# Optimization experiments

Measured on AMD Instinct MI355X. Metric: run time of the kernel, lower is better.

Reference implementation:

```python
import jax, jax.numpy as jnp
import numpy as np

TOP_K = 2
EPS = 1e-9


def setup_inputs() -> dict:
    key = jax.random.key(0)
    k1, k2, k3, k4 = jax.random.split(key, 4)
    B, T, D, H, E = 4, 2048, 1024, 4096, 8
    x = jax.random.normal(k1, (B, T, D), dtype=jnp.float32)
    Wr = jax.random.normal(k2, (D, E), dtype=jnp.float32) * 0.02
    W1 = jax.random.normal(k3, (E, D, H), dtype=jnp.float32) * 0.02
    W2 = jax.random.normal(k4, (E, H, D), dtype=jnp.float32) * 0.02
    return {"x": x, "Wr": Wr, "W1": W1, "W2": W2}


def reference(x, Wr, W1, W2):
    # x: (B,T,D); Wr: (D,E); W1: (E,D,H); W2: (E,H,D)
    E = Wr.shape[1]
    logits = jnp.einsum('btd,de->bte', x, Wr)          # (B,T,E)
    probs = jax.nn.softmax(logits, axis=-1)
    top_p, top_i = jax.lax.top_k(probs, TOP_K)         # (B,T,K)
    gates = top_p / (jnp.sum(top_p, axis=-1, keepdims=True) + EPS)
    # combine weights per expert: (B,T,E), zero where expert not selected
    oh = jax.nn.one_hot(top_i, E, dtype=x.dtype)       # (B,T,K,E)
    comb = jnp.sum(oh * gates[..., None], axis=2)      # (B,T,E)
    out = jnp.zeros_like(x)
    for e in range(E):  # fixed small expert loop
        h = jax.nn.gelu(jnp.einsum('btd,dh->bth', x, W1[e]), approximate=False)
        y = jnp.einsum('bth,hd->btd', h, W2[e])
        out = out + comb[..., e:e + 1] * y
    # load-balancing loss (on detached stats, matching torch .detach())
    mask = (jnp.sum(oh, axis=2) > 0).astype(jnp.float32)  # (B,T,E)
    imp = jnp.sum(jax.lax.stop_gradient(probs), axis=(0, 1))
    load = jnp.sum(jax.lax.stop_gradient(mask), axis=(0, 1))
    imp = imp / (jnp.sum(imp) + EPS)
    load = load / (jnp.sum(load) + EPS)
    lb = jnp.sum(imp * load) * E
    return out, lb
```

## Files before the change

kernel.cpp:

```cpp
#include <hip/hip_runtime.h>
#include <hip/hip_bf16.h>
#include <math.h>

#define NTOK 8192
#define DDIM 1024
#define HDIM 4096
#define NEXP 8
#define HROWS (NTOK*2 + 128)
#define RBLK 512

typedef unsigned int u32;
typedef unsigned short u16;
typedef __bf16 bf16x8 __attribute__((ext_vector_type(8)));
typedef float f32x4 __attribute__((ext_vector_type(4)));
typedef u16 u16x8 __attribute__((ext_vector_type(8)));
typedef u16 u16x4 __attribute__((ext_vector_type(4)));

__device__ __forceinline__ u16 f2bf(float f){
  u32 u = __builtin_bit_cast(u32, f);
  u32 r = (u + 0x7FFFu + ((u >> 16) & 1u)) >> 16;
  return (u16)r;
}
__device__ __forceinline__ float bf2f(u16 b){
  u32 u = ((u32)b) << 16;
  return __builtin_bit_cast(float, u);
}
__device__ __forceinline__ void gl_lds16(const void* g, void* l){
  __builtin_amdgcn_global_load_lds(
      (const __attribute__((address_space(1))) u32*)g,
      (__attribute__((address_space(3))) u32*)l, 16, 0, 0);
}

__global__ __launch_bounds__(256) void cvtx_kernel(const float* __restrict__ x,
                                                   u16* __restrict__ xb){
  long i = (long)(blockIdx.x * 256 + threadIdx.x) * 8;
  float4 a = *(const float4*)(x + i);
  float4 b = *(const float4*)(x + i + 4);
  u16x8 o;
  o[0]=f2bf(a.x); o[1]=f2bf(a.y); o[2]=f2bf(a.z); o[3]=f2bf(a.w);
  o[4]=f2bf(b.x); o[5]=f2bf(b.y); o[6]=f2bf(b.z); o[7]=f2bf(b.w);
  *(u16x8*)(xb + i) = o;
}

__global__ __launch_bounds__(256) void transpose_cvt(const float* __restrict__ in,
                                                     u16* __restrict__ out,
                                                     int R, int C){
  int e = blockIdx.z;
  const float* pin = in + (long)e * R * C;
  u16* pout = out + (long)e * R * C;
  __shared__ u16 tile[64][65];
  int c0 = blockIdx.x * 64, r0 = blockIdx.y * 64;
  int tid = threadIdx.x;
#pragma unroll
  for (int j = 0; j < 16; j++){
    int idx = tid + 256 * j;
    int r = idx >> 6, c = idx & 63;
    tile[r][c] = f2bf(pin[(long)(r0 + r) * C + c0 + c]);
  }
  __syncthreads();
#pragma unroll
  for (int j = 0; j < 16; j++){
    int idx = tid + 256 * j;
    int r = idx >> 6, c = idx & 63;
    pout[(long)(c0 + r) * R + r0 + c] = tile[c][r];
  }
}

__global__ __launch_bounds__(1024) void route_kernel(const float* __restrict__ x,
                                                     const float* __restrict__ Wr,
                                                     int4* __restrict__ meta,
                                                     float2* __restrict__ gates,
                                                     int* __restrict__ selrk,
                                                     int* __restrict__ blockhist,
                                                     float* __restrict__ impPart){
  const int wid = threadIdx.x >> 6;
  const int lane = threadIdx.x & 63;
  const int t = blockIdx.x * 16 + wid;
  const float* xr = x + (long)t * DDIM;
  float acc[NEXP] = {};
  for (int d0 = lane * 4; d0 < DDIM; d0 += 256){
    float4 xv = *(const float4*)(xr + d0);
    const float* w = Wr + d0 * NEXP;
#pragma unroll
    for (int q = 0; q < 4; q++){
      float xq = ((const float*)&xv)[q];
      float4 w0 = *(const float4*)(w + q * NEXP);
      float4 w1 = *(const float4*)(w + q * NEXP + 4);
      acc[0] += xq * w0.x; acc[1] += xq * w0.y; acc[2] += xq * w0.z; acc[3] += xq * w0.w;
      acc[4] += xq * w1.x; acc[5] += xq * w1.y; acc[6] += xq * w1.z; acc[7] += xq * w1.w;
    }
  }
#pragma unroll
  for (int e = 0; e < NEXP; e++){
#pragma unroll
    for (int off = 32; off; off >>= 1) acc[e] += __shfl_xor(acc[e], off, 64);
  }
  __shared__ int sel_s[32];
  __shared__ float p_s[16][NEXP];
  if (lane == 0){
    float mx = acc[0];
#pragma unroll
    for (int e = 1; e < NEXP; e++) mx = fmaxf(mx, acc[e]);
    float p[NEXP]; float s = 0.f;
#pragma unroll
    for (int e = 0; e < NEXP; e++){ p[e] = expf(acc[e] - mx); s += p[e]; }
    float inv = 1.f / s;
#pragma unroll
    for (int e = 0; e < NEXP; e++){ p[e] *= inv; p_s[wid][e] = p[e]; }
    int i0 = 0; float v0 = p[0];
#pragma unroll
    for (int e = 1; e < NEXP; e++) if (p[e] > v0){ v0 = p[e]; i0 = e; }
    int i1 = -1; float v1 = -1.f;
#pragma unroll
    for (int e = 0; e < NEXP; e++) if (e != i0 && p[e] > v1){ v1 = p[e]; i1 = e; }
    float gs = v0 + v1 + 1e-9f;
    meta[t] = make_int4(i0, i1, 0, 0);
    gates[t] = make_float2(v0 / gs, v1 / gs);
    sel_s[wid * 2] = i0;
    sel_s[wid * 2 + 1] = i1;
  }
  __syncthreads();
  const int tid = threadIdx.x;
  if (tid < 32){
    int e = sel_s[tid];
    int r = 0;
    for (int m = 0; m < tid; m++) r += (sel_s[m] == e) ? 1 : 0;
    selrk[blockIdx.x * 32 + tid] = (r << 3) | e;
  }
  if (tid < NEXP){
    int hcount = 0;
#pragma unroll
    for (int m = 0; m < 32; m++) hcount += (sel_s[m] == tid) ? 1 : 0;
    blockhist[blockIdx.x * NEXP + tid] = hcount;
    float s = 0.f;
#pragma unroll
    for (int w = 0; w < 16; w++) s += p_s[w][tid];
    impPart[blockIdx.x * NEXP + tid] = s;
  }
}

__global__ __launch_bounds__(512) void scan_kernel(int* __restrict__ blockhist,
                                                   const float* __restrict__ impPart,
                                                   int* __restrict__ cnt,
                                                   int* __restrict__ offs,
                                                   float* __restrict__ imp){
  const int e = threadIdx.x >> 6;
  const int lane = threadIdx.x & 63;
  const int base = lane * 8;
  int v[8]; int s = 0;
#pragma unroll
  for (int i = 0; i < 8; i++){
    int tmp = blockhist[(base + i) * NEXP + e];
    v[i] = s; s += tmp;
  }
  int inc = s;
#pragma unroll
  for (int off = 1; off < 64; off <<= 1){
    int o = __shfl_up(inc, off, 64);
    if (lane >= off) inc += o;
  }
  int excl = inc - s;
#pragma unroll
  for (int i = 0; i < 8; i++) blockhist[(base + i) * NEXP + e] = v[i] + excl;
  int tot = __shfl(inc, 63, 64);
  float fs = 0.f;
#pragma unroll
  for (int i = 0; i < 8; i++) fs += impPart[(base + i) * NEXP + e];
#pragma unroll
  for (int off = 32; off; off >>= 1) fs += __shfl_xor(fs, off, 64);
  __shared__ int cnt_s[NEXP];
  if (lane == 0){ cnt_s[e] = tot; cnt[e] = tot; imp[e] = fs; }
  __syncthreads();
  if (threadIdx.x == 0){
    int o = 0;
    for (int q = 0; q < NEXP; q++){ offs[q] = o; o += cnt_s[q]; }
  }
}

__global__ __launch_bounds__(256) void fill_kernel(const int* __restrict__ selrk,
                                                   const int* __restrict__ blockhist,
                                                   int* __restrict__ elist,
                                                   int4* __restrict__ meta){
  int m = blockIdx.x * 256 + threadIdx.x;
  int t = m >> 1, c = m & 1, b = m >> 5;
  int pk = selrk[m];
  int e = pk & 7, r = pk >> 3;
  int gslot = blockhist[b * NEXP + e] + r;
  elist[e * NTOK + gslot] = t;
  ((int*)meta)[t * 4 + 2 + c] = gslot;
}

__global__ __launch_bounds__(256) void gemm1_kernel(const u16* __restrict__ xb,
                                                    const u16* __restrict__ w1t,
                                                    u16* __restrict__ h,
                                                    const int* __restrict__ elist,
                                                    const int* __restrict__ cnt,
                                                    const int* __restrict__ offs){
  const int e = blockIdx.z;
  const int n_e = cnt[e];
  const int tt = blockIdx.y;
  if (tt * 128 >= n_e) return;
  const int hb = blockIdx.x * 128;
  __shared__ __align__(16) u16 As[128 * 64];
  __shared__ __align__(16) u16 Bs[128 * 64];
  const int tid = threadIdx.x;
  const int colb = (tid & 7) * 8;
  long agb[4]; int arow[4];
#pragma unroll
  for (int q = 0; q < 4; q++){
    int row = q * 32 + (tid >> 3);
    int slot = tt * 128 + row;
    int sl = slot < n_e ? slot : n_e - 1;
    int tok = elist[e * NTOK + sl];
    arow[q] = row;
    agb[q] = (long)tok * DDIM + colb;
  }
  const long bgb = ((long)e * HDIM + hb) * DDIM;
  const int wid = tid >> 6, lane = tid & 63;
  const int wr = (wid >> 1) * 64, wc = (wid & 1) * 64;
  const int fr = lane & 15, fq = lane >> 4;
  f32x4 acc[4][4] = {};
  for (int kb = 0; kb < DDIM; kb += 64){
    __syncthreads();
#pragma unroll
    for (int q = 0; q < 4; q++){
      int row = q * 32 + (tid >> 3);
      gl_lds16(xb + agb[q] + kb, &As[arow[q] * 64 + colb]);
      gl_lds16(w1t + bgb + (long)row * DDIM + kb + colb, &Bs[row * 64 + colb]);
    }
    __syncthreads();
#pragma unroll
    for (int kk = 0; kk < 2; kk++){
      bf16x8 af[4], bfr[4];
#pragma unroll
      for (int m = 0; m < 4; m++) af[m] = *(const bf16x8*)&As[(wr + m * 16 + fr) * 64 + kk * 32 + fq * 8];
#pragma unroll
      for (int n = 0; n < 4; n++) bfr[n] = *(const bf16x8*)&Bs[(wc + n * 16 + fr) * 64 + kk * 32 + fq * 8];
#pragma unroll
      for (int m = 0; m < 4; m++)
#pragma unroll
        for (int n = 0; n < 4; n++)
          acc[m][n] = __builtin_amdgcn_mfma_f32_16x16x32_bf16(af[m], bfr[n], acc[m][n], 0, 0, 0);
    }
  }
  const int hrow0 = offs[e] + tt * 128;
#pragma unroll
  for (int m = 0; m < 4; m++){
#pragma unroll
    for (int j = 0; j < 4; j++){
      int row = wr + m * 16 + fq * 4 + j;
      int slot = tt * 128 + row;
      if (slot >= n_e) continue;
      long base = (long)(hrow0 + row) * HDIM + hb + wc;
#pragma unroll
      for (int n = 0; n < 4; n++){
        float v = acc[m][n][j];
        v = 0.5f * v * (1.0f + erff(v * 0.70710678118f));
        h[base + n * 16 + fr] = f2bf(v);
      }
    }
  }
}

__global__ __launch_bounds__(256) void gemm2_kernel(const u16* __restrict__ h,
                                                    const u16* __restrict__ w2t,
                                                    u16* __restrict__ ypair,
                                                    const int* __restrict__ cnt,
                                                    const int* __restrict__ offs){
  const int e = blockIdx.z;
  const int n_e = cnt[e];
  const int tt = blockIdx.y;
  if (tt * 128 >= n_e) return;
  const int db = blockIdx.x * 128;
  __shared__ __align__(16) u16 As[128 * 64];
  __shared__ __align__(16) u16 Bs[128 * 64];
  const int tid = threadIdx.x;
  const int colb = (tid & 7) * 8;
  const long arow0 = (long)(offs[e] + tt * 128);
  const long bgb = ((long)e * DDIM + db) * HDIM;
  const int wid = tid >> 6, lane = tid & 63;
  const int wr = (wid >> 1) * 64, wc = (wid & 1) * 64;
  const int fr = lane & 15, fq = lane >> 4;
  f32x4 acc[4][4] = {};
  for (int kb = 0; kb < HDIM; kb += 64){
    __syncthreads();
#pragma unroll
    for (int q = 0; q < 4; q++){
      int row = q * 32 + (tid >> 3);
      gl_lds16(h + (arow0 + row) * HDIM + kb + colb, &As[row * 64 + colb]);
      gl_lds16(w2t + bgb + (long)row * HDIM + kb + colb, &Bs[row * 64 + colb]);
    }
    __syncthreads();
#pragma unroll
    for (int kk = 0; kk < 2; kk++){
      bf16x8 af[4], bfr[4];
#pragma unroll
      for (int m = 0; m < 4; m++) af[m] = *(const bf16x8*)&As[(wr + m * 16 + fr) * 64 + kk * 32 + fq * 8];
#pragma unroll
      for (int n = 0; n < 4; n++) bfr[n] = *(const bf16x8*)&Bs[(wc + n * 16 + fr) * 64 + kk * 32 + fq * 8];
#pragma unroll
      for (int m = 0; m < 4; m++)
#pragma unroll
        for (int n = 0; n < 4; n++)
          acc[m][n] = __builtin_amdgcn_mfma_f32_16x16x32_bf16(af[m], bfr[n], acc[m][n], 0, 0, 0);
    }
  }
  const long prow0 = arow0;
#pragma unroll
  for (int m = 0; m < 4; m++){
#pragma unroll
    for (int j = 0; j < 4; j++){
      int row = wr + m * 16 + fq * 4 + j;
      int slot = tt * 128 + row;
      if (slot >= n_e) continue;
      long base = (prow0 + row) * DDIM + db + wc;
#pragma unroll
      for (int n = 0; n < 4; n++) ypair[base + n * 16 + fr] = f2bf(acc[m][n][j]);
    }
  }
}

__global__ __launch_bounds__(256) void combine_kernel(const u16* __restrict__ ypair,
                                                      const int4* __restrict__ meta,
                                                      const float2* __restrict__ gates,
                                                      const int* __restrict__ offs,
                                                      float* __restrict__ out){
  int t = blockIdx.x;
  int c = threadIdx.x;
  int4 m = meta[t];
  float2 g = gates[t];
  long p0 = (long)(offs[m.x] + m.z) * DDIM + c * 4;
  long p1 = (long)(offs[m.y] + m.w) * DDIM + c * 4;
  u16x4 y0 = *(const u16x4*)&ypair[p0];
  u16x4 y1 = *(const u16x4*)&ypair[p1];
  float4 o;
  o.x = g.x * bf2f(y0[0]) + g.y * bf2f(y1[0]);
  o.y = g.x * bf2f(y0[1]) + g.y * bf2f(y1[1]);
  o.z = g.x * bf2f(y0[2]) + g.y * bf2f(y1[2]);
  o.w = g.x * bf2f(y0[3]) + g.y * bf2f(y1[3]);
  *(float4*)&out[(long)t * DDIM + c * 4] = o;
}

__global__ void lb_kernel(const float* __restrict__ imp, const int* __restrict__ cnt,
                          float* __restrict__ outp){
  if (threadIdx.x == 0 && blockIdx.x == 0){
    float si = 0.f, sl = 0.f;
    for (int e = 0; e < NEXP; e++){ si += imp[e]; sl += (float)cnt[e]; }
    float lb = 0.f;
    for (int e = 0; e < NEXP; e++)
      lb += (imp[e] / (si + 1e-9f)) * ((float)cnt[e] / (sl + 1e-9f));
    outp[0] = lb * (float)NEXP;
  }
}

extern "C" void kernel_launch(void* const* d_in, const int* in_sizes, int n_in,
                              void* d_out, int out_size, void* d_ws, size_t ws_size,
                              hipStream_t stream){
  const float* x  = (const float*)d_in[0];
  const float* Wr = (const float*)d_in[1];
  const float* W1 = (const float*)d_in[2];
  const float* W2 = (const float*)d_in[3];
  float* out = (float*)d_out;
  char* ws = (char*)d_ws;
  size_t off = 0;
  u16* xb = (u16*)(ws + off);   off += (size_t)NTOK * DDIM * 2;
  u16* wt = (u16*)(ws + off);   off += (size_t)NEXP * DDIM * HDIM * 2;
  u16* h  = (u16*)(ws + off);   off += (size_t)HROWS * HDIM * 2;
  u16* yp = (u16*)(ws + off);   off += (size_t)NTOK * 2 * DDIM * 2;
  int* elist    = (int*)(ws + off);    off += (size_t)NEXP * NTOK * 4;
  int4* meta    = (int4*)(ws + off);   off += (size_t)NTOK * 16;
  float2* gts   = (float2*)(ws + off); off += (size_t)NTOK * 8;
  int* selrk    = (int*)(ws + off);    off += (size_t)NTOK * 2 * 4;
  int* bhist    = (int*)(ws + off);    off += (size_t)RBLK * NEXP * 4;
  float* impP   = (float*)(ws + off);  off += (size_t)RBLK * NEXP * 4;
  int* cnt      = (int*)(ws + off);    off += 32;
  float* imp    = (float*)(ws + off);  off += 32;
  int* offs     = (int*)(ws + off);    off += 32;
  if (ws_size < off) return;

  cvtx_kernel<<<4096, 256, 0, stream>>>(x, xb);
  route_kernel<<<RBLK, 1024, 0, stream>>>(x, Wr, meta, gts, selrk, bhist, impP);
  scan_kernel<<<1, 512, 0, stream>>>(bhist, impP, cnt, offs, imp);
  fill_kernel<<<NTOK * 2 / 256, 256, 0, stream>>>(selrk, bhist, elist, meta);
  transpose_cvt<<<dim3(HDIM / 64, DDIM / 64, NEXP), 256, 0, stream>>>(W1, wt, DDIM, HDIM);
  gemm1_kernel<<<dim3(HDIM / 128, NTOK / 128, NEXP), 256, 0, stream>>>(xb, wt, h, elist, cnt, offs);
  transpose_cvt<<<dim3(DDIM / 64, HDIM / 64, NEXP), 256, 0, stream>>>(W2, wt, HDIM, DDIM);
  gemm2_kernel<<<dim3(DDIM / 128, NTOK / 128, NEXP), 256, 0, stream>>>(h, wt, yp, cnt, offs);
  combine_kernel<<<NTOK, 256, 0, stream>>>(yp, meta, gts, offs, out);
  lb_kernel<<<1, 64, 0, stream>>>(imp, cnt, out + (size_t)NTOK * DDIM);
}
```

Measured before the change: 598.7 us.

## Double-buffer LDS, swizzle shared tiles, and remap grid for XCD locality in GEMMs

Both expert GEMM kernels now prefetch the next K tile into a second LDS buffer while computing on the current one, dropping one barrier per iteration. LDS columns are XOR-swizzled by row so that fragment reads avoid bank conflicts. The 3D grid is flattened and remapped so consecutive blocks on each XCD work on the same expert and on nearby token and column tiles, to improve L2 reuse. LDS usage doubles, which may lower occupancy.

```diff
diff --git a/kernel.cpp b/kernel.cpp
--- a/kernel.cpp
+++ b/kernel.cpp
@@ -196,52 +196,73 @@
                                                     const int* __restrict__ elist,
                                                     const int* __restrict__ cnt,
                                                     const int* __restrict__ offs){
-  const int e = blockIdx.z;
+  const int NDB = HDIM / 128;
+  const int NTT = NTOK / 128;
+  const int nloc = NDB * NTT;
+  const int nwg = NEXP * nloc;
+  int bid = blockIdx.x;
+  int nb = (bid & 7) * (nwg >> 3) + (bid >> 3);
+  const int e = nb / nloc;
+  int le = nb % nloc;
+  int tti = le & 3;
+  int db  = (le >> 2) % NDB;
+  int tg  = le / (4 * NDB);
+  int tt  = tg * 4 + tti;
   const int n_e = cnt[e];
-  const int tt = blockIdx.y;
   if (tt * 128 >= n_e) return;
-  const int hb = blockIdx.x * 128;
-  __shared__ __align__(16) u16 As[128 * 64];
-  __shared__ __align__(16) u16 Bs[128 * 64];
+  const int hb = db * 128;
+  __shared__ __align__(16) u16 As[2][128 * 64];
+  __shared__ __align__(16) u16 Bs[2][128 * 64];
   const int tid = threadIdx.x;
-  const int colb = (tid & 7) * 8;
-  long agb[4]; int arow[4];
+  const int csrc = (((tid & 7) ^ ((tid >> 3) & 7)) << 3);
+  const int clin = (tid & 7) << 3;
+  long agb[4], bga[4]; int lrow[4];
+  const long bgb = ((long)e * HDIM + hb) * DDIM;
 #pragma unroll
   for (int q = 0; q < 4; q++){
     int row = q * 32 + (tid >> 3);
     int slot = tt * 128 + row;
     int sl = slot < n_e ? slot : n_e - 1;
     int tok = elist[e * NTOK + sl];
-    arow[q] = row;
-    agb[q] = (long)tok * DDIM + colb;
-  }
-  const long bgb = ((long)e * HDIM + hb) * DDIM;
+    lrow[q] = row;
+    agb[q] = (long)tok * DDIM + csrc;
+    bga[q] = bgb + (long)row * DDIM + csrc;
+  }
   const int wid = tid >> 6, lane = tid & 63;
   const int wr = (wid >> 1) * 64, wc = (wid & 1) * 64;
   const int fr = lane & 15, fq = lane >> 4;
   f32x4 acc[4][4] = {};
+#pragma unroll
+  for (int q = 0; q < 4; q++){
+    gl_lds16(xb + agb[q], &As[0][lrow[q] * 64 + clin]);
+    gl_lds16(w1t + bga[q], &Bs[0][lrow[q] * 64 + clin]);
+  }
+  __syncthreads();
+  int cur = 0;
   for (int kb = 0; kb < DDIM; kb += 64){
-    __syncthreads();
-#pragma unroll
-    for (int q = 0; q < 4; q++){
-      int row = q * 32 + (tid >> 3);
-      gl_lds16(xb + agb[q] + kb, &As[arow[q] * 64 + colb]);
-      gl_lds16(w1t + bgb + (long)row * DDIM + kb + colb, &Bs[row * 64 + colb]);
-    }
-    __syncthreads();
+    if (kb + 64 < DDIM){
+#pragma unroll
+      for (int q = 0; q < 4; q++){
+        gl_lds16(xb + agb[q] + kb + 64, &As[cur ^ 1][lrow[q] * 64 + clin]);
+        gl_lds16(w1t + bga[q] + kb + 64, &Bs[cur ^ 1][lrow[q] * 64 + clin]);
+      }
+    }
 #pragma unroll
     for (int kk = 0; kk < 2; kk++){
+      const int coff = (((kk * 4 + fq) ^ (fr & 7)) << 3);
       bf16x8 af[4], bfr[4];
 #pragma unroll
-      for (int m = 0; m < 4; m++) af[m] = *(const bf16x8*)&As[(wr + m * 16 + fr) * 64 + kk * 32 + fq * 8];
-#pragma unroll
-      for (int n = 0; n < 4; n++) bfr[n] = *(const bf16x8*)&Bs[(wc + n * 16 + fr) * 64 + kk * 32 + fq * 8];
+      for (int m = 0; m < 4; m++) af[m] = *(const bf16x8*)&As[cur][(wr + m * 16 + fr) * 64 + coff];
+#pragma unroll
+      for (int n = 0; n < 4; n++) bfr[n] = *(const bf16x8*)&Bs[cur][(wc + n * 16 + fr) * 64 + coff];
 #pragma unroll
       for (int m = 0; m < 4; m++)
 #pragma unroll
         for (int n = 0; n < 4; n++)
           acc[m][n] = __builtin_amdgcn_mfma_f32_16x16x32_bf16(af[m], bfr[n], acc[m][n], 0, 0, 0);
     }
+    __syncthreads();
+    cur ^= 1;
   }
   const int hrow0 = offs[e] + tt * 128;
 #pragma unroll
@@ -267,45 +288,72 @@
                                                     u16* __restrict__ ypair,
                                                     const int* __restrict__ cnt,
                                                     const int* __restrict__ offs){
-  const int e = blockIdx.z;
+  const int NDB = DDIM / 128;
+  const int NTT = NTOK / 128;
+  const int nloc = NDB * NTT;
+  const int nwg = NEXP * nloc;
+  int bid = blockIdx.x;
+  int nb = (bid & 7) * (nwg >> 3) + (bid >> 3);
+  const int e = nb / nloc;
+  int le = nb % nloc;
+  int tti = le & 3;
+  int db  = (le >> 2) % NDB;
+  int tg  = le / (4 * NDB);
+  int tt  = tg * 4 + tti;
   const int n_e = cnt[e];
-  const int tt = blockIdx.y;
   if (tt * 128 >= n_e) return;
-  const int db = blockIdx.x * 128;
-  __shared__ __align__(16) u16 As[128 * 64];
-  __shared__ __align__(16) u16 Bs[128 * 64];
+  const int dbb = db * 128;
+  __shared__ __align__(16) u16 As[2][128 * 64];
+  __shared__ __align__(16) u16 Bs[2][128 * 64];
   const int tid = threadIdx.x;
-  const int colb = (tid & 7) * 8;
+  const int csrc = (((tid & 7) ^ ((tid >> 3) & 7)) << 3);
+  const int clin = (tid & 7) << 3;
   const long arow0 = (long)(offs[e] + tt * 128);
-  const long bgb = ((long)e * DDIM + db) * HDIM;
+  const long bgb = ((long)e * DDIM + dbb) * HDIM;
+  long aga[4], bga[4]; int lrow[4];
+#pragma unroll
+  for (int q = 0; q < 4; q++){
+    int row = q * 32 + (tid >> 3);
+    lrow[q] = row;
+    aga[q] = (arow0 + row) * HDIM + csrc;
+    bga[q] = bgb + (long)row * HDIM + csrc;
+  }
   const int wid = tid >> 6, lane = tid & 63;
   const int wr = (wid >> 1) * 64, wc = (wid & 1) * 64;
   const int fr = lane & 15, fq = lane >> 4;
   f32x4 acc[4][4] = {};
+#pragma unroll
+  for (int q = 0; q < 4; q++){
+    gl_lds16(h + aga[q], &As[0][lrow[q] * 64 + clin]);
+    gl_lds16(w2t + bga[q], &Bs[0][lrow[q] * 64 + clin]);
+  }
+  __syncthreads();
+  int cur = 0;
   for (int kb = 0; kb < HDIM; kb += 64){
-    __syncthreads();
-#pragma unroll
-    for (int q = 0; q < 4; q++){
-      int row = q * 32 + (tid >> 3);
-      gl_lds16(h + (arow0 + row) * HDIM + kb + colb, &As[row * 64 + colb]);
-      gl_lds16(w2t + bgb + (long)row * HDIM + kb + colb, &Bs[row * 64 + colb]);
-    }
-    __syncthreads();
+    if (kb + 64 < HDIM){
+#pragma unroll
+      for (int q = 0; q < 4; q++){
+        gl_lds16(h + aga[q] + kb + 64, &As[cur ^ 1][lrow[q] * 64 + clin]);
+        gl_lds16(w2t + bga[q] + kb + 64, &Bs[cur ^ 1][lrow[q] * 64 + clin]);
+      }
+    }
 #pragma unroll
     for (int kk = 0; kk < 2; kk++){
+      const int coff = (((kk * 4 + fq) ^ (fr & 7)) << 3);
       bf16x8 af[4], bfr[4];
 #pragma unroll
-      for (int m = 0; m < 4; m++) af[m] = *(const bf16x8*)&As[(wr + m * 16 + fr) * 64 + kk * 32 + fq * 8];
-#pragma unroll
-      for (int n = 0; n < 4; n++) bfr[n] = *(const bf16x8*)&Bs[(wc + n * 16 + fr) * 64 + kk * 32 + fq * 8];
+      for (int m = 0; m < 4; m++) af[m] = *(const bf16x8*)&As[cur][(wr + m * 16 + fr) * 64 + coff];
+#pragma unroll
+      for (int n = 0; n < 4; n++) bfr[n] = *(const bf16x8*)&Bs[cur][(wc + n * 16 + fr) * 64 + coff];
 #pragma unroll
       for (int m = 0; m < 4; m++)
 #pragma unroll
         for (int n = 0; n < 4; n++)
           acc[m][n] = __builtin_amdgcn_mfma_f32_16x16x32_bf16(af[m], bfr[n], acc[m][n], 0, 0, 0);
     }
-  }
-  const long prow0 = arow0;
+    __syncthreads();
+    cur ^= 1;
+  }
 #pragma unroll
   for (int m = 0; m < 4; m++){
 #pragma unroll
@@ -313,7 +361,7 @@
       int row = wr + m * 16 + fq * 4 + j;
       int slot = tt * 128 + row;
       if (slot >= n_e) continue;
-      long base = (prow0 + row) * DDIM + db + wc;
+      long base = (arow0 + row) * DDIM + dbb + wc;
 #pragma unroll
       for (int n = 0; n < 4; n++) ypair[base + n * 16 + fr] = f2bf(acc[m][n][j]);
     }
@@ -383,9 +431,9 @@
   scan_kernel<<<1, 512, 0, stream>>>(bhist, impP, cnt, offs, imp);
   fill_kernel<<<NTOK * 2 / 256, 256, 0, stream>>>(selrk, bhist, elist, meta);
   transpose_cvt<<<dim3(HDIM / 64, DDIM / 64, NEXP), 256, 0, stream>>>(W1, wt, DDIM, HDIM);
-  gemm1_kernel<<<dim3(HDIM / 128, NTOK / 128, NEXP), 256, 0, stream>>>(xb, wt, h, elist, cnt, offs);
+  gemm1_kernel<<<NEXP * (NTOK / 128) * (HDIM / 128), 256, 0, stream>>>(xb, wt, h, elist, cnt, offs);
   transpose_cvt<<<dim3(DDIM / 64, HDIM / 64, NEXP), 256, 0, stream>>>(W2, wt, HDIM, DDIM);
-  gemm2_kernel<<<dim3(DDIM / 128, NTOK / 128, NEXP), 256, 0, stream>>>(h, wt, yp, cnt, offs);
+  gemm2_kernel<<<NEXP * (NTOK / 128) * (DDIM / 128), 256, 0, stream>>>(h, wt, yp, cnt, offs);
   combine_kernel<<<NTOK, 256, 0, stream>>>(yp, meta, gts, offs, out);
   lb_kernel<<<1, 64, 0, stream>>>(imp, cnt, out + (size_t)NTOK * DDIM);
 }
```

Result: slower. 675.7 us (+12.9%).

## Replace expert GEMMs with 256x256 double-buffered swizzled 8-wave MFMA kernel

Applied to the files above, without the earlier changes.

Both expert GEMMs now go through one templated kernel with 256x256 output tiles, 512 threads and double-buffered LDS prefetching two K-steps ahead. Explicit vmcnt waits and raw barriers replace full __syncthreads. It also XOR-swizzles LDS chunks to avoid bank conflicts and raises wave priority around the MFMA bursts. The aim is more data reuse per tile and overlap of global loads with MFMA work, at the cost of 128KB LDS (one block per CU), more padding waste for small experts, and fragile hand-written wait counts.

```diff
diff --git a/kernel.cpp b/kernel.cpp
--- a/kernel.cpp
+++ b/kernel.cpp
@@ -6,7 +6,7 @@
 #define DDIM 1024
 #define HDIM 4096
 #define NEXP 8
-#define HROWS (NTOK*2 + 128)
+#define HROWS (NTOK*2 + 256)
 #define RBLK 512
 
 typedef unsigned int u32;
@@ -16,6 +16,12 @@
 typedef u16 u16x8 __attribute__((ext_vector_type(8)));
 typedef u16 u16x4 __attribute__((ext_vector_type(4)));
 
+#define SCHEDB __builtin_amdgcn_sched_barrier(0)
+#define BARR   __builtin_amdgcn_s_barrier()
+#define LGKM0  asm volatile("s_waitcnt lgkmcnt(0)" ::: "memory")
+#define VMC8   asm volatile("s_waitcnt vmcnt(8)" ::: "memory")
+#define VMC0   asm volatile("s_waitcnt vmcnt(0)" ::: "memory")
+
 __device__ __forceinline__ u16 f2bf(float f){
   u32 u = __builtin_bit_cast(u32, f);
   u32 r = (u + 0x7FFFu + ((u >> 16) & 1u)) >> 16;
@@ -29,6 +35,10 @@
   __builtin_amdgcn_global_load_lds(
       (const __attribute__((address_space(1))) u32*)g,
       (__attribute__((address_space(3))) u32*)l, 16, 0, 0);
+}
+__device__ __forceinline__ bf16x8 ldsrd(const u16* base, int r, int kk, int fq, int fr){
+  int chunk = (kk * 4 + fq) ^ (fr & 7);
+  return *(const bf16x8*)&base[r * 64 + chunk * 8];
 }
 
 __global__ __launch_bounds__(256) void cvtx_kernel(const float* __restrict__ x,
@@ -190,132 +200,156 @@
   ((int*)meta)[t * 4 + 2 + c] = gslot;
 }
 
-__global__ __launch_bounds__(256) void gemm1_kernel(const u16* __restrict__ xb,
-                                                    const u16* __restrict__ w1t,
-                                                    u16* __restrict__ h,
-                                                    const int* __restrict__ elist,
-                                                    const int* __restrict__ cnt,
-                                                    const int* __restrict__ offs){
-  const int e = blockIdx.z;
+template<int KD, int ND, bool GATHER, bool GELU>
+__global__ __launch_bounds__(512) void gemm8p_kernel(const u16* __restrict__ Ag,
+                                                     const u16* __restrict__ Bg,
+                                                     u16* __restrict__ Cg,
+                                                     const int* __restrict__ elist,
+                                                     const int* __restrict__ cnt,
+                                                     const int* __restrict__ offs){
+  const int NBT = ND / 256;
+  const int nloc = 32 * NBT;
+  const int e  = blockIdx.x / nloc;
+  const int rr = blockIdx.x % nloc;
+  const int nb = rr / 32;
+  const int tt = rr % 32;
   const int n_e = cnt[e];
-  const int tt = blockIdx.y;
-  if (tt * 128 >= n_e) return;
-  const int hb = blockIdx.x * 128;
-  __shared__ __align__(16) u16 As[128 * 64];
-  __shared__ __align__(16) u16 Bs[128 * 64];
+  if (tt * 256 >= n_e) return;
+
+  __shared__ __align__(16) u16 As[2][256 * 64];
+  __shared__ __align__(16) u16 Bs[2][256 * 64];
+
   const int tid = threadIdx.x;
-  const int colb = (tid & 7) * 8;
-  long agb[4]; int arow[4];
-#pragma unroll
-  for (int q = 0; q < 4; q++){
-    int row = q * 32 + (tid >> 3);
-    int slot = tt * 128 + row;
-    int sl = slot < n_e ? slot : n_e - 1;
-    int tok = elist[e * NTOK + sl];
-    arow[q] = row;
-    agb[q] = (long)tok * DDIM + colb;
-  }
-  const long bgb = ((long)e * HDIM + hb) * DDIM;
-  const int wid = tid >> 6, lane = tid & 63;
-  const int wr = (wid >> 1) * 64, wc = (wid & 1) * 64;
-  const int fr = lane & 15, fq = lane >> 4;
-  f32x4 acc[4][4] = {};
-  for (int kb = 0; kb < DDIM; kb += 64){
-    __syncthreads();
-#pragma unroll
-    for (int q = 0; q < 4; q++){
-      int row = q * 32 + (tid >> 3);
-      gl_lds16(xb + agb[q] + kb, &As[arow[q] * 64 + colb]);
-      gl_lds16(w1t + bgb + (long)row * DDIM + kb + colb, &Bs[row * 64 + colb]);
+  const int w = tid >> 6, l = tid & 63;
+  const int wm = w >> 2, wn = w & 3;
+  const int wrow = wm * 128, wcol = wn * 64;
+  const int fr = l & 15, fq = l >> 4;
+  const int chunk = (l & 7) ^ ((l >> 3) & 7);
+  const int row0 = offs[e] + tt * 256;
+
+  int srcA[4], srcB[4], ldsO[4];
+#pragma unroll
+  for (int i = 0; i < 4; i++){
+    int rowg = i * 64 + w * 8 + (l >> 3);
+    int arow;
+    if (GATHER){
+      int slot = tt * 256 + rowg;
+      if (slot >= n_e) slot = n_e - 1;
+      arow = elist[e * NTOK + slot];
+    } else {
+      arow = row0 + rowg;
     }
-    __syncthreads();
-#pragma unroll
-    for (int kk = 0; kk < 2; kk++){
-      bf16x8 af[4], bfr[4];
-#pragma unroll
-      for (int m = 0; m < 4; m++) af[m] = *(const bf16x8*)&As[(wr + m * 16 + fr) * 64 + kk * 32 + fq * 8];
-#pragma unroll
-      for (int n = 0; n < 4; n++) bfr[n] = *(const bf16x8*)&Bs[(wc + n * 16 + fr) * 64 + kk * 32 + fq * 8];
+    srcA[i] = arow * KD + chunk * 8;
+    srcB[i] = (e * ND + nb * 256 + rowg) * KD + chunk * 8;
+    ldsO[i] = rowg * 64 + (l & 7) * 8;
+  }
+
+  const int NKT = KD / 64;
+  f32x4 acc[8][4] = {};
+
+#pragma unroll
+  for (int i = 0; i < 4; i++){
+    gl_lds16(Ag + srcA[i], &As[0][ldsO[i]]);
+    gl_lds16(Bg + srcB[i], &Bs[0][ldsO[i]]);
+  }
+#pragma unroll
+  for (int i = 0; i < 4; i++){
+    gl_lds16(Ag + srcA[i] + 64, &As[1][ldsO[i]]);
+    gl_lds16(Bg + srcB[i] + 64, &Bs[1][ldsO[i]]);
+  }
+  SCHEDB; VMC8; SCHEDB; BARR; SCHEDB;
+
+  for (int t = 0; t < NKT; ++t){
+    const int p = t & 1;
+    const u16* Ap = &As[p][0];
+    const u16* Bp = &Bs[p][0];
+    bf16x8 a[4][2], b0[2][2], b1[2][2];
+#pragma unroll
+    for (int m = 0; m < 4; m++)
+#pragma unroll
+      for (int kk = 0; kk < 2; kk++)
+        a[m][kk] = ldsrd(Ap, wrow + m * 16 + fr, kk, fq, fr);
+#pragma unroll
+    for (int n = 0; n < 2; n++)
+#pragma unroll
+      for (int kk = 0; kk < 2; kk++)
+        b0[n][kk] = ldsrd(Bp, wcol + n * 16 + fr, kk, fq, fr);
+    __builtin_amdgcn_s_setprio(1);
+#pragma unroll
+    for (int kk = 0; kk < 2; kk++)
 #pragma unroll
       for (int m = 0; m < 4; m++)
 #pragma unroll
-        for (int n = 0; n < 4; n++)
-          acc[m][n] = __builtin_amdgcn_mfma_f32_16x16x32_bf16(af[m], bfr[n], acc[m][n], 0, 0, 0);
+        for (int n = 0; n < 2; n++)
+          acc[m][n] = __builtin_amdgcn_mfma_f32_16x16x32_bf16(a[m][kk], b0[n][kk], acc[m][n], 0, 0, 0);
+    __builtin_amdgcn_s_setprio(0);
+#pragma unroll
+    for (int n = 0; n < 2; n++)
+#pragma unroll
+      for (int kk = 0; kk < 2; kk++)
+        b1[n][kk] = ldsrd(Bp, wcol + 32 + n * 16 + fr, kk, fq, fr);
+    __builtin_amdgcn_s_setprio(1);
+#pragma unroll
+    for (int kk = 0; kk < 2; kk++)
+#pragma unroll
+      for (int m = 0; m < 4; m++)
+#pragma unroll
+        for (int n = 0; n < 2; n++)
+          acc[m][2 + n] = __builtin_amdgcn_mfma_f32_16x16x32_bf16(a[m][kk], b1[n][kk], acc[m][2 + n], 0, 0, 0);
+    __builtin_amdgcn_s_setprio(0);
+#pragma unroll
+    for (int m = 0; m < 4; m++)
+#pragma unroll
+      for (int kk = 0; kk < 2; kk++)
+        a[m][kk] = ldsrd(Ap, wrow + 64 + m * 16 + fr, kk, fq, fr);
+    __builtin_amdgcn_s_setprio(1);
+#pragma unroll
+    for (int kk = 0; kk < 2; kk++)
+#pragma unroll
+      for (int m = 0; m < 4; m++)
+#pragma unroll
+        for (int n = 0; n < 2; n++)
+          acc[4 + m][n] = __builtin_amdgcn_mfma_f32_16x16x32_bf16(a[m][kk], b0[n][kk], acc[4 + m][n], 0, 0, 0);
+    __builtin_amdgcn_s_setprio(0);
+    LGKM0; SCHEDB; BARR; SCHEDB;
+    if (t + 2 < NKT){
+      const int kb = (t + 2) * 64;
+#pragma unroll
+      for (int i = 0; i < 4; i++){
+        gl_lds16(Ag + srcA[i] + kb, &As[p][ldsO[i]]);
+        gl_lds16(Bg + srcB[i] + kb, &Bs[p][ldsO[i]]);
+      }
     }
-  }
-  const int hrow0 = offs[e] + tt * 128;
-#pragma unroll
-  for (int m = 0; m < 4; m++){
+    __builtin_amdgcn_s_setprio(1);
+#pragma unroll
+    for (int kk = 0; kk < 2; kk++)
+#pragma unroll
+      for (int m = 0; m < 4; m++)
+#pragma unroll
+        for (int n = 0; n < 2; n++)
+          acc[4 + m][2 + n] = __builtin_amdgcn_mfma_f32_16x16x32_bf16(a[m][kk], b1[n][kk], acc[4 + m][2 + n], 0, 0, 0);
+    __builtin_amdgcn_s_setprio(0);
+    if (t + 1 < NKT){
+      SCHEDB;
+      if (t + 2 < NKT) { VMC8; } else { VMC0; }
+      SCHEDB; BARR; SCHEDB;
+    }
+  }
+
+  const int c0 = nb * 256 + wcol;
+#pragma unroll
+  for (int m = 0; m < 8; m++){
 #pragma unroll
     for (int j = 0; j < 4; j++){
-      int row = wr + m * 16 + fq * 4 + j;
-      int slot = tt * 128 + row;
+      int slot = tt * 256 + wrow + m * 16 + fq * 4 + j;
       if (slot >= n_e) continue;
-      long base = (long)(hrow0 + row) * HDIM + hb + wc;
+      long base = (long)(offs[e] + slot) * ND + c0;
 #pragma unroll
       for (int n = 0; n < 4; n++){
         float v = acc[m][n][j];
-        v = 0.5f * v * (1.0f + erff(v * 0.70710678118f));
-        h[base + n * 16 + fr] = f2bf(v);
+        if (GELU) v = 0.5f * v * (1.0f + erff(v * 0.70710678118f));
+        Cg[base + n * 16 + fr] = f2bf(v);
       }
-    }
-  }
-}
-
-__global__ __launch_bounds__(256) void gemm2_kernel(const u16* __restrict__ h,
-                                                    const u16* __restrict__ w2t,
-                                                    u16* __restrict__ ypair,
-                                                    const int* __restrict__ cnt,
-                                                    const int* __restrict__ offs){
-  const int e = blockIdx.z;
-  const int n_e = cnt[e];
-  const int tt = blockIdx.y;
-  if (tt * 128 >= n_e) return;
-  const int db = blockIdx.x * 128;
-  __shared__ __align__(16) u16 As[128 * 64];
-  __shared__ __align__(16) u16 Bs[128 * 64];
-  const int tid = threadIdx.x;
-  const int colb = (tid & 7) * 8;
-  const long arow0 = (long)(offs[e] + tt * 128);
-  const long bgb = ((long)e * DDIM + db) * HDIM;
-  const int wid = tid >> 6, lane = tid & 63;
-  const int wr = (wid >> 1) * 64, wc = (wid & 1) * 64;
-  const int fr = lane & 15, fq = lane >> 4;
-  f32x4 acc[4][4] = {};
-  for (int kb = 0; kb < HDIM; kb += 64){
-    __syncthreads();
-#pragma unroll
-    for (int q = 0; q < 4; q++){
-      int row = q * 32 + (tid >> 3);
-      gl_lds16(h + (arow0 + row) * HDIM + kb + colb, &As[row * 64 + colb]);
-      gl_lds16(w2t + bgb + (long)row * HDIM + kb + colb, &Bs[row * 64 + colb]);
-    }
-    __syncthreads();
-#pragma unroll
-    for (int kk = 0; kk < 2; kk++){
-      bf16x8 af[4], bfr[4];
-#pragma unroll
-      for (int m = 0; m < 4; m++) af[m] = *(const bf16x8*)&As[(wr + m * 16 + fr) * 64 + kk * 32 + fq * 8];
-#pragma unroll
-      for (int n = 0; n < 4; n++) bfr[n] = *(const bf16x8*)&Bs[(wc + n * 16 + fr) * 64 + kk * 32 + fq * 8];
-#pragma unroll
-      for (int m = 0; m < 4; m++)
-#pragma unroll
-        for (int n = 0; n < 4; n++)
-          acc[m][n] = __builtin_amdgcn_mfma_f32_16x16x32_bf16(af[m], bfr[n], acc[m][n], 0, 0, 0);
-    }
-  }
-  const long prow0 = arow0;
-#pragma unroll
-  for (int m = 0; m < 4; m++){
-#pragma unroll
-    for (int j = 0; j < 4; j++){
-      int row = wr + m * 16 + fq * 4 + j;
-      int slot = tt * 128 + row;
-      if (slot >= n_e) continue;
-      long base = (prow0 + row) * DDIM + db + wc;
-#pragma unroll
-      for (int n = 0; n < 4; n++) ypair[base + n * 16 + fr] = f2bf(acc[m][n][j]);
     }
   }
 }
@@ -383,9 +417,11 @@
   scan_kernel<<<1, 512, 0, stream>>>(bhist, impP, cnt, offs, imp);
   fill_kernel<<<NTOK * 2 / 256, 256, 0, stream>>>(selrk, bhist, elist, meta);
   transpose_cvt<<<dim3(HDIM / 64, DDIM / 64, NEXP), 256, 0, stream>>>(W1, wt, DDIM, HDIM);
-  gemm1_kernel<<<dim3(HDIM / 128, NTOK / 128, NEXP), 256, 0, stream>>>(xb, wt, h, elist, cnt, offs);
+  gemm8p_kernel<DDIM, HDIM, true, true><<<NEXP * 32 * (HDIM / 256), 512, 0, stream>>>(
+      xb, wt, h, elist, cnt, offs);
   transpose_cvt<<<dim3(DDIM / 64, HDIM / 64, NEXP), 256, 0, stream>>>(W2, wt, HDIM, DDIM);
-  gemm2_kernel<<<dim3(DDIM / 128, NTOK / 128, NEXP), 256, 0, stream>>>(h, wt, yp, cnt, offs);
+  gemm8p_kernel<HDIM, DDIM, false, false><<<NEXP * 32 * (DDIM / 256), 512, 0, stream>>>(
+      h, wt, yp, elist, cnt, offs);
   combine_kernel<<<NTOK, 256, 0, stream>>>(yp, meta, gts, offs, out);
   lb_kernel<<<1, 64, 0, stream>>>(imp, cnt, out + (size_t)NTOK * DDIM);
 }
```

Measured after the change: 1.387 ms. 132% more time.
